# Performance work log

Measured on AMD Instinct MI355X. Metric: run time of the kernel, lower is better.

The kernel has to match this reference:

```python
import jax, jax.numpy as jnp
import numpy as np

NUM_EMBED = 8192
EMBED_DIM = 256


def setup_inputs() -> dict:
    key = jax.random.key(0)
    k1, k2 = jax.random.split(key)
    input_data = jax.random.normal(k1, (32, EMBED_DIM, 32, 32), dtype=jnp.float32)
    codebook = jax.random.normal(k2, (NUM_EMBED, EMBED_DIM), dtype=jnp.float32)
    return {"input_data": input_data, "codebook": codebook}


def reference(input_data, codebook):
    N, C, H, W = input_data.shape
    # NCHW -> NHWC -> [N*H*W, C]
    data = jnp.transpose(input_data, (0, 2, 3, 1)).reshape(-1, C)
    dist = (
        jnp.sum(data * data, axis=1, keepdims=True)          # [T, 1]
        - 2.0 * jnp.einsum("tc,kc->tk", data, codebook)      # [T, K]
        + jnp.sum(codebook * codebook, axis=1)[None, :]       # [1, K]
    )
    embed_ind = jnp.argmin(dist, axis=1)                      # [T]
    quantize = codebook[embed_ind]                            # [T, C] gather
    quantize_detach = data + jax.lax.stop_gradient(quantize - data)
    return quantize, quantize_detach, data
```

## Files before the change

kernel.cpp:

```cpp
#include <hip/hip_runtime.h>
#include <stdint.h>


#define T_TOT 32768
#define K_TOT 8192
#define CD    256
#define SPLITS 4
#define NSPLIT 2048
#define MT    64
#define NTI   32

typedef _Float16 h8 __attribute__((ext_vector_type(8)));
typedef _Float16 h4 __attribute__((ext_vector_type(4)));
typedef float f4 __attribute__((ext_vector_type(4)));
typedef unsigned long long u64;
typedef unsigned int u32;

#define WS_AP    0u
#define WS_BP    16777216u
#define WS_E2    20971520u
#define WS_E2B   21004288u
#define WS_CAND  21037056u
#define WS_NEED  23265280u

__device__ __forceinline__ u64 shfl_xor_u64(u64 v, int off, int w) {
  unsigned lo = (unsigned)v, hi = (unsigned)(v >> 32);
  lo = __shfl_xor(lo, off, w);
  hi = __shfl_xor(hi, off, w);
  return ((u64)hi << 32) | lo;
}
__device__ __forceinline__ u64 umin64(u64 a, u64 b) { return a < b ? a : b; }
__device__ __forceinline__ u64 umax64(u64 a, u64 b) { return a < b ? b : a; }
__device__ __forceinline__ u32 umin32(u32 a, u32 b) { return a < b ? a : b; }
__device__ __forceinline__ u32 umax32(u32 a, u32 b) { return a < b ? b : a; }

__device__ __forceinline__ void gll16(const void* g, void* l) {
  __builtin_amdgcn_global_load_lds(
      (const __attribute__((address_space(1))) void*)g,
      (__attribute__((address_space(3))) void*)l, 16, 0, 0);
}

__device__ __forceinline__ void stage_b(const _Float16* __restrict__ gsrc,
                                        _Float16* ldst, int lane) {
  #pragma unroll
  for (int kk = 0; kk < 8; ++kk)
    gll16(gsrc + kk * 512 + lane * 8, ldst + kk * 512);
}



__global__ __launch_bounds__(256) void cvt_data_kernel(
    const float* __restrict__ in, _Float16* __restrict__ Ap,
    float* __restrict__ out3) {
  __shared__ float Ds[32][257];
  const int tid = threadIdx.x;
  const int t0 = blockIdx.x * 32;
  const int nbase = (t0 >> 10) << 18;
  const int tin = t0 & 1023;
  #pragma unroll
  for (int p = 0; p < 8; ++p) {
    const int id = p * 256 + tid;
    const int cc = id >> 3, t4 = (id & 7) * 4;
    const float4 v = *(const float4*)(in + nbase + cc * 1024 + tin + t4);
    Ds[t4 + 0][cc] = v.x;
    Ds[t4 + 1][cc] = v.y;
    Ds[t4 + 2][cc] = v.z;
    Ds[t4 + 3][cc] = v.w;
  }
  __syncthreads();
  const u64 g0 = (u64)(t0 >> 4);
  #pragma unroll
  for (int p = 0; p < 4; ++p) {
    const int id = p * 256 + tid;
    const int gl = id >> 9, kk = (id >> 6) & 7, l = id & 63;
    const int row = gl * 16 + (l & 15);
    const int c0 = kk * 32 + (l >> 4) * 8;
    h8 hv;
    #pragma unroll
    for (int j = 0; j < 8; ++j) hv[j] = (_Float16)(-Ds[row][c0 + j]);
    *(h8*)(Ap + ((g0 + (u64)gl) * 8 + kk) * 512 + (u64)l * 8) = hv;
  }
  #pragma unroll 8
  for (int tt = 0; tt < 32; ++tt)
    out3[(u64)(t0 + tt) * CD + tid] = Ds[tt][tid];
}

__global__ __launch_bounds__(256) void cvt_cb_kernel(
    const float* __restrict__ cb, _Float16* __restrict__ Bp,
    float* __restrict__ e2, float* __restrict__ e2b) {
  __shared__ float Cs[16][260];
  const int tid = threadIdx.x;
  const int g = blockIdx.x;
  #pragma unroll
  for (int r = 0; r < 16; ++r)
    Cs[r][tid] = cb[((u64)g * 16 + r) * 256 + tid];
  __syncthreads();
  const int w = tid >> 6, lane = tid & 63;
  #pragma unroll
  for (int rr = 0; rr < 4; ++rr) {
    const int row = w * 4 + rr;
    const float4 v = *(const float4*)&Cs[row][lane * 4];
    float s = v.x * v.x + v.y * v.y + v.z * v.z + v.w * v.w;
    #pragma unroll
    for (int off = 32; off >= 1; off >>= 1) s += __shfl_xor(s, off, 64);
    if (lane == 0) {
      e2[g * 16 + row] = s;
      e2b[g * 16 + row] = 0.5f * s + 256.0f;
    }
  }
  #pragma unroll
  for (int p = 0; p < 2; ++p) {
    const int id = p * 256 + tid;
    const int kk = id >> 6, l = id & 63;
    const int row = l & 15, c0 = kk * 32 + (l >> 4) * 8;
    h8 hv;
    #pragma unroll
    for (int j = 0; j < 8; ++j) hv[j] = (_Float16)Cs[row][c0 + j];
    *(h8*)(Bp + ((u64)g * 8 + kk) * 512 + (u64)l * 8) = hv;
  }
}

__global__ __launch_bounds__(256, 2) void screen_kernel(
    const _Float16* __restrict__ Ap, const _Float16* __restrict__ Bp,
    const float* __restrict__ e2b, u64* __restrict__ cand) {
  __shared__ __align__(16) _Float16 bsm[4][2][4096];
  __shared__ __align__(16) float e2s[2048];

  const int tid = threadIdx.x;
  const int lane = tid & 63;
  const int w = __builtin_amdgcn_readfirstlane(tid >> 6);
  const int q = lane >> 4;
  const int c15 = lane & 15;

  const int x = blockIdx.x & 7;
  const int m = blockIdx.x >> 3;
  const int split = x >> 1;
  const int bm = m * 2 + (x & 1);
  const int t0 = bm * MT;
  const int n0s = split * NSPLIT;

  const h8* ap = (const h8*)Ap + (u64)(t0 >> 4) * 512 + lane;
  h8 af[4][8];
  #pragma unroll
  for (int mi = 0; mi < 4; ++mi)
    #pragma unroll
    for (int kk = 0; kk < 8; ++kk)
      af[mi][kk] = ap[(mi * 8 + kk) * 64];

  const _Float16* bg = Bp + ((u64)(n0s >> 4) + (u64)w) * 4096;
  stage_b(bg, &bsm[w][0][0], lane);
  stage_b(bg + 16384, &bsm[w][1][0], lane);
  gll16(e2b + n0s + w * 512 + lane * 4, e2s + w * 512);
  gll16(e2b + n0s + w * 512 + 256 + lane * 4, e2s + w * 512 + 256);

  u32 m1[16], m2[16];
  #pragma unroll
  for (int r = 0; r < 16; ++r) { m1[r] = 0xffffffffu; m2[r] = 0xffffffffu; }

  __syncthreads();

  #pragma unroll 2
  for (int nt = 0; nt < NTI; ++nt) {
    asm volatile("s_waitcnt vmcnt(8)" ::: "memory");
    _Float16* slot = &bsm[w][nt & 1][0];
    const float ev = e2s[nt * 64 + w * 16 + c15];
    h8 bf[8];
    #pragma unroll
    for (int kk = 0; kk < 8; ++kk)
      bf[kk] = *(const h8*)(slot + kk * 512 + lane * 8);

    f4 acc[4];
    #pragma unroll
    for (int mi = 0; mi < 4; ++mi) acc[mi] = (f4){ev, ev, ev, ev};
    __builtin_amdgcn_s_setprio(1);
    #pragma unroll
    for (int kk = 0; kk < 8; ++kk) {
      acc[0] = __builtin_amdgcn_mfma_f32_16x16x32_f16(af[0][kk], bf[kk], acc[0], 0, 0, 0);
      acc[1] = __builtin_amdgcn_mfma_f32_16x16x32_f16(af[1][kk], bf[kk], acc[1], 0, 0, 0);
      acc[2] = __builtin_amdgcn_mfma_f32_16x16x32_f16(af[2][kk], bf[kk], acc[2], 0, 0, 0);
      acc[3] = __builtin_amdgcn_mfma_f32_16x16x32_f16(af[3][kk], bf[kk], acc[3], 0, 0, 0);
    }
    __builtin_amdgcn_s_setprio(0);

    asm volatile("s_waitcnt lgkmcnt(0)" ::: "memory");
    __builtin_amdgcn_sched_barrier(0);
    const int g2 = (nt + 2 < NTI) ? nt + 2 : NTI - 1;
    stage_b(bg + (u64)g2 * 16384, slot, lane);

    #pragma unroll
    for (int mi = 0; mi < 4; ++mi)
      #pragma unroll
      for (int reg = 0; reg < 4; ++reg) {
        const int r = mi * 4 + reg;
        const u32 k = (__float_as_uint(acc[mi][reg]) & ~63u) | (u32)nt;
        const u32 hi = umax32(m1[r], k);
        m1[r] = umin32(m1[r], k);
        m2[r] = umin32(m2[r], hi);
      }
  }

  u64 P1[16], P2[16];
  #pragma unroll
  for (int r = 0; r < 16; ++r) {
    const u32 l1 = m1[r] & 63u, l2 = m2[r] & 63u;
    const u32 col1 = (u32)(n0s + (int)l1 * 64 + w * 16 + c15);
    const u32 col2 = (u32)(n0s + (int)l2 * 64 + w * 16 + c15);
    P1[r] = ((u64)m1[r] << 32) | col1;
    P2[r] = ((u64)m2[r] << 32) | col2;
  }
  #pragma unroll
  for (int st = 1; st < 16; st <<= 1) {
    #pragma unroll
    for (int r = 0; r < 16; ++r) {
      const u64 o1 = shfl_xor_u64(P1[r], st, 16);
      const u64 o2 = shfl_xor_u64(P2[r], st, 16);
      const u64 n1 = umin64(P1[r], o1);
      const u64 hi = umax64(P1[r], o1);
      P2[r] = umin64(hi, umin64(P2[r], o2));
      P1[r] = n1;
    }
  }
  __syncthreads();
  u64* mb = (u64*)&bsm[0][0][0];
  if (c15 == 0) {
    #pragma unroll
    for (int r = 0; r < 16; ++r) {
      const int mi = r >> 2, reg = r & 3;
      const int row = mi * 16 + q * 4 + reg;
      mb[(w * 64 + row) * 2 + 0] = P1[r];
      mb[(w * 64 + row) * 2 + 1] = P2[r];
    }
  }
  __syncthreads();
  if (tid < 64) {
    const u64 a1 = mb[(0 * 64 + tid) * 2], a2 = mb[(0 * 64 + tid) * 2 + 1];
    const u64 b1 = mb[(1 * 64 + tid) * 2], b2 = mb[(1 * 64 + tid) * 2 + 1];
    const u64 c1 = mb[(2 * 64 + tid) * 2], c2 = mb[(2 * 64 + tid) * 2 + 1];
    const u64 d1 = mb[(3 * 64 + tid) * 2], d2 = mb[(3 * 64 + tid) * 2 + 1];
    const u64 x1 = umin64(a1, b1);
    const u64 x2 = umin64(umax64(a1, b1), umin64(a2, b2));
    const u64 y1 = umin64(c1, d1);
    const u64 y2 = umin64(umax64(c1, d1), umin64(c2, d2));
    const u64 n1 = umin64(x1, y1);
    const u64 n2 = umin64(umax64(x1, y1), umin64(x2, y2));
    cand[(u64)(t0 + tid) * 8 + split * 2 + 0] = n1;
    cand[(u64)(t0 + tid) * 8 + split * 2 + 1] = n2;
  }
}

__global__ __launch_bounds__(256) void rescore_output_kernel(
    const float* __restrict__ cb, const float* __restrict__ e2,
    const u64* __restrict__ cand, float* __restrict__ out) {
  const int tid = threadIdx.x;
  const int w = tid >> 6, lane = tid & 63;
  const int t0 = blockIdx.x * 32 + w * 8;
  float* out1 = out;
  float* out2 = out + 8388608;
  const float* out3 = out + 16777216;
  #pragma unroll 1
  for (int s = 0; s < 8; ++s) {
    const int t = t0 + s;
    int colv = 0;
    if (lane < 8) colv = (int)(u32)cand[(u64)t * 8 + lane];
    const float4 x = *(const float4*)(out3 + (u64)t * CD + lane * 4);
    float bestd = 1e30f; int bestc = 0x7fffffff;
    #pragma unroll
    for (int j = 0; j < 8; ++j) {
      const int col = __shfl(colv, j, 64);
      const float4 e = *(const float4*)(cb + (u64)col * CD + lane * 4);
      float p4 = x.x * e.x + x.y * e.y + x.z * e.z + x.w * e.w;
      #pragma unroll
      for (int off = 32; off >= 1; off >>= 1) p4 += __shfl_xor(p4, off, 64);
      const float d = e2[col] - 2.0f * p4;
      if (d < bestd || (d == bestd && col < bestc)) { bestd = d; bestc = col; }
    }
    const float4 q4 = *(const float4*)(cb + (u64)bestc * CD + lane * 4);
    float4 qd4;
    qd4.x = x.x + (q4.x - x.x);
    qd4.y = x.y + (q4.y - x.y);
    qd4.z = x.z + (q4.z - x.z);
    qd4.w = x.w + (q4.w - x.w);
    const u64 o = (u64)t * CD + lane * 4;
    *(float4*)(out1 + o) = q4;
    *(float4*)(out2 + o) = qd4;
  }
}


__global__ __launch_bounds__(256) void norms_kernel(const float* __restrict__ in,
                                                    const float* __restrict__ cb,
                                                    float* __restrict__ e2,
                                                    float* __restrict__ x2) {
  const int b = blockIdx.x;
  const int tid = threadIdx.x;
  if (b < 2048) {
    const int wave = tid >> 6, lane = tid & 63;
    const int row = b * 4 + wave;
    const float4 v = *(const float4*)(cb + row * CD + lane * 4);
    float s = v.x * v.x + v.y * v.y + v.z * v.z + v.w * v.w;
    #pragma unroll
    for (int off = 32; off >= 1; off >>= 1) s += __shfl_down(s, off, 64);
    if (lane == 0) e2[row] = s;
  } else {
    const int t = (b - 2048) * 256 + tid;
    const float* p = in + ((t >> 10) << 18) + (t & 1023);
    float s = 0.f;
    #pragma unroll 8
    for (int c = 0; c < CD; ++c) { const float v = p[c << 10]; s += v * v; }
    x2[t] = s;
  }
}

__global__ __launch_bounds__(256) void dist_argmin_kernel(
    const float* __restrict__ in, const float* __restrict__ cb,
    const float* __restrict__ e2, const float* __restrict__ x2,
    u64* __restrict__ packed) {
  __shared__ __align__(16) float As_[32][128];
  __shared__ __align__(16) float Bs_[32][128];
  const int tid = threadIdx.x;
  const int tx = tid & 15, ty = tid >> 4;
  const int tb = blockIdx.x & 255;
  const int ks = blockIdx.x >> 8;
  const int t0 = tb * 128;
  const int nbase = (t0 >> 10) << 18;
  const int tin = t0 & 1023;
  float xi[8];
  #pragma unroll
  for (int i = 0; i < 8; ++i)
    xi[i] = x2[t0 + ty * 4 + (i & 3) + ((i >> 2) << 6)];
  u64 best[8];
  #pragma unroll
  for (int i = 0; i < 8; ++i) best[i] = ~0ull;
  for (int kt = 0; kt < 32; ++kt) {
    const int k0 = ks * 4096 + kt * 128;
    float acc[8][8];
    #pragma unroll
    for (int i = 0; i < 8; ++i)
      #pragma unroll
      for (int j = 0; j < 8; ++j) acc[i][j] = 0.f;
    float ej[8];
    #pragma unroll
    for (int j = 0; j < 8; ++j)
      ej[j] = e2[k0 + tx * 4 + (j & 3) + ((j >> 2) << 6)];
    for (int ch = 0; ch < 8; ++ch) {
      const int c0 = ch * 32;
      #pragma unroll
      for (int p = 0; p < 4; ++p) {
        const int l = p * 1024 + tid * 4;
        const int cc = l >> 7, tt = l & 127;
        *(float4*)&As_[cc][tt] =
            *(const float4*)(in + nbase + (c0 + cc) * 1024 + tin + tt);
      }
      #pragma unroll
      for (int p = 0; p < 4; ++p) {
        const int ix = p * 256 + tid;
        const int kk = ix >> 3, cs = (ix & 7) * 4;
        const float4 v = *(const float4*)(cb + (k0 + kk) * CD + c0 + cs);
        Bs_[cs + 0][kk] = v.x; Bs_[cs + 1][kk] = v.y;
        Bs_[cs + 2][kk] = v.z; Bs_[cs + 3][kk] = v.w;
      }
      __syncthreads();
      #pragma unroll
      for (int cc = 0; cc < 32; ++cc) {
        const float4 a0 = *(const float4*)&As_[cc][ty * 4];
        const float4 a1 = *(const float4*)&As_[cc][64 + ty * 4];
        const float4 b0 = *(const float4*)&Bs_[cc][tx * 4];
        const float4 b1 = *(const float4*)&Bs_[cc][64 + tx * 4];
        const float a[8]  = {a0.x, a0.y, a0.z, a0.w, a1.x, a1.y, a1.z, a1.w};
        const float bb[8] = {b0.x, b0.y, b0.z, b0.w, b1.x, b1.y, b1.z, b1.w};
        #pragma unroll
        for (int i = 0; i < 8; ++i)
          #pragma unroll
          for (int j = 0; j < 8; ++j)
            acc[i][j] += a[i] * bb[j];
      }
      __syncthreads();
    }
    #pragma unroll
    for (int i = 0; i < 8; ++i) {
      u64 m = best[i];
      #pragma unroll
      for (int j = 0; j < 8; ++j) {
        const float dist = (xi[i] - 2.0f * acc[i][j]) + ej[j];
        const int kidx = k0 + tx * 4 + (j & 3) + ((j >> 2) << 6);
        const u64 pk = ((u64)__float_as_uint(dist) << 32) | (unsigned)kidx;
        m = pk < m ? pk : m;
      }
      best[i] = m;
    }
  }
  #pragma unroll
  for (int i = 0; i < 8; ++i) {
    u64 m = best[i];
    #pragma unroll
    for (int off = 8; off >= 1; off >>= 1) {
      const u64 o = shfl_xor_u64(m, off, 16);
      m = o < m ? o : m;
    }
    if (tx == 0)
      atomicMin(&packed[t0 + ty * 4 + (i & 3) + ((i >> 2) << 6)], m);
  }
}

__global__ __launch_bounds__(256) void output_kernel(
    const float* __restrict__ in, const float* __restrict__ cb,
    const u64* __restrict__ packed, float* __restrict__ out) {
  __shared__ float Ds[32][257];
  __shared__ int idxs[32];
  const int tid = threadIdx.x;
  const int t0 = blockIdx.x * 32;
  const int nbase = (t0 >> 10) << 18;
  const int tin = t0 & 1023;
  if (tid < 32) idxs[tid] = (int)(packed[t0 + tid] & 0xffffffffull);
  #pragma unroll 8
  for (int p = 0; p < 32; ++p) {
    const int lin = p * 256 + tid;
    const int cc = lin >> 5, tt = lin & 31;
    Ds[tt][cc] = in[nbase + cc * 1024 + tin + tt];
  }
  __syncthreads();
  float* out1 = out;
  float* out2 = out + 8388608;
  float* out3 = out + 16777216;
  for (int tt = 0; tt < 32; ++tt) {
    const float d = Ds[tt][tid];
    const int k = idxs[tt];
    const float q = cb[k * CD + tid];
    const float qd = d + (q - d);
    const int o = (t0 + tt) * CD + tid;
    out1[o] = q;
    out2[o] = qd;
    out3[o] = d;
  }
}

extern "C" void kernel_launch(void* const* d_in, const int* in_sizes, int n_in,
                              void* d_out, int out_size, void* d_ws, size_t ws_size,
                              hipStream_t stream) {
  const float* in = (const float*)d_in[0];
  const float* cb = (const float*)d_in[1];
  float* out = (float*)d_out;

  if (ws_size >= WS_NEED) {
    _Float16* Ap = (_Float16*)((char*)d_ws + WS_AP);
    _Float16* Bp = (_Float16*)((char*)d_ws + WS_BP);
    float* e2  = (float*)((char*)d_ws + WS_E2);
    float* e2b = (float*)((char*)d_ws + WS_E2B);
    u64* cand  = (u64*)((char*)d_ws + WS_CAND);
    float* out3 = out + 16777216;

    cvt_data_kernel<<<T_TOT / 32, 256, 0, stream>>>(in, Ap, out3);
    cvt_cb_kernel<<<K_TOT / 16, 256, 0, stream>>>(cb, Bp, e2, e2b);
    screen_kernel<<<(T_TOT / MT) * SPLITS, 256, 0, stream>>>(Ap, Bp, e2b, cand);
    rescore_output_kernel<<<T_TOT / 32, 256, 0, stream>>>(cb, e2, cand, out);
  } else {
    u64* packed = (u64*)d_ws;
    float* e2 = (float*)((char*)d_ws + 262144);
    float* x2 = (float*)((char*)d_ws + 294912);
    (void)hipMemsetAsync(packed, 0xFF, T_TOT * sizeof(u64), stream);
    norms_kernel<<<2176, 256, 0, stream>>>(in, cb, e2, x2);
    dist_argmin_kernel<<<512, 256, 0, stream>>>(in, cb, e2, x2, packed);
    output_kernel<<<T_TOT / 32, 256, 0, stream>>>(in, cb, packed, out);
  }
}
```

Before: 329.7 us.

## Merge prep kernels and fuse rescore into screen via last-block counter

The two conversion kernels become one launch whose blocks split into data-transpose and codebook-conversion roles. The separate rescore/output kernel is removed: each screen block bumps a per-row-tile atomic counter, and the last of the four split blocks for that tile re-scores the candidates and writes the outputs. This cuts launches and inter-kernel gaps, at the cost of a memset for the counters, extra fences, and the rescore tail running on only a quarter of the screen blocks.

```diff
diff --git a/kernel.cpp b/kernel.cpp
--- a/kernel.cpp
+++ b/kernel.cpp
@@ -11,7 +11,6 @@
 #define NTI   32
 
 typedef _Float16 h8 __attribute__((ext_vector_type(8)));
-typedef _Float16 h4 __attribute__((ext_vector_type(4)));
 typedef float f4 __attribute__((ext_vector_type(4)));
 typedef unsigned long long u64;
 typedef unsigned int u32;
@@ -21,6 +20,7 @@
 #define WS_E2    20971520u
 #define WS_E2B   21004288u
 #define WS_CAND  21037056u
+#define WS_CTR   23134208u
 #define WS_NEED  23265280u
 
 __device__ __forceinline__ u64 shfl_xor_u64(u64 v, int off, int w) {
@@ -49,82 +49,84 @@
 
 
 
-__global__ __launch_bounds__(256) void cvt_data_kernel(
-    const float* __restrict__ in, _Float16* __restrict__ Ap,
+__global__ __launch_bounds__(256) void prep_kernel(
+    const float* __restrict__ in, const float* __restrict__ cb,
+    _Float16* __restrict__ Ap, _Float16* __restrict__ Bp,
+    float* __restrict__ e2, float* __restrict__ e2b,
     float* __restrict__ out3) {
-  __shared__ float Ds[32][257];
+  __shared__ float S[32][257];
   const int tid = threadIdx.x;
-  const int t0 = blockIdx.x * 32;
-  const int nbase = (t0 >> 10) << 18;
-  const int tin = t0 & 1023;
-  #pragma unroll
-  for (int p = 0; p < 8; ++p) {
-    const int id = p * 256 + tid;
-    const int cc = id >> 3, t4 = (id & 7) * 4;
-    const float4 v = *(const float4*)(in + nbase + cc * 1024 + tin + t4);
-    Ds[t4 + 0][cc] = v.x;
-    Ds[t4 + 1][cc] = v.y;
-    Ds[t4 + 2][cc] = v.z;
-    Ds[t4 + 3][cc] = v.w;
-  }
-  __syncthreads();
-  const u64 g0 = (u64)(t0 >> 4);
-  #pragma unroll
-  for (int p = 0; p < 4; ++p) {
-    const int id = p * 256 + tid;
-    const int gl = id >> 9, kk = (id >> 6) & 7, l = id & 63;
-    const int row = gl * 16 + (l & 15);
-    const int c0 = kk * 32 + (l >> 4) * 8;
-    h8 hv;
-    #pragma unroll
-    for (int j = 0; j < 8; ++j) hv[j] = (_Float16)(-Ds[row][c0 + j]);
-    *(h8*)(Ap + ((g0 + (u64)gl) * 8 + kk) * 512 + (u64)l * 8) = hv;
-  }
-  #pragma unroll 8
-  for (int tt = 0; tt < 32; ++tt)
-    out3[(u64)(t0 + tt) * CD + tid] = Ds[tt][tid];
-}
-
-__global__ __launch_bounds__(256) void cvt_cb_kernel(
-    const float* __restrict__ cb, _Float16* __restrict__ Bp,
-    float* __restrict__ e2, float* __restrict__ e2b) {
-  __shared__ float Cs[16][260];
-  const int tid = threadIdx.x;
-  const int g = blockIdx.x;
-  #pragma unroll
-  for (int r = 0; r < 16; ++r)
-    Cs[r][tid] = cb[((u64)g * 16 + r) * 256 + tid];
-  __syncthreads();
-  const int w = tid >> 6, lane = tid & 63;
-  #pragma unroll
-  for (int rr = 0; rr < 4; ++rr) {
-    const int row = w * 4 + rr;
-    const float4 v = *(const float4*)&Cs[row][lane * 4];
-    float s = v.x * v.x + v.y * v.y + v.z * v.z + v.w * v.w;
-    #pragma unroll
-    for (int off = 32; off >= 1; off >>= 1) s += __shfl_xor(s, off, 64);
-    if (lane == 0) {
-      e2[g * 16 + row] = s;
-      e2b[g * 16 + row] = 0.5f * s + 256.0f;
-    }
-  }
-  #pragma unroll
-  for (int p = 0; p < 2; ++p) {
-    const int id = p * 256 + tid;
-    const int kk = id >> 6, l = id & 63;
-    const int row = l & 15, c0 = kk * 32 + (l >> 4) * 8;
-    h8 hv;
-    #pragma unroll
-    for (int j = 0; j < 8; ++j) hv[j] = (_Float16)Cs[row][c0 + j];
-    *(h8*)(Bp + ((u64)g * 8 + kk) * 512 + (u64)l * 8) = hv;
+  if (blockIdx.x < 1024) {
+    const int t0 = blockIdx.x * 32;
+    const int nbase = (t0 >> 10) << 18;
+    const int tin = t0 & 1023;
+    #pragma unroll
+    for (int p = 0; p < 8; ++p) {
+      const int id = p * 256 + tid;
+      const int cc = id >> 3, t4 = (id & 7) * 4;
+      const float4 v = *(const float4*)(in + nbase + cc * 1024 + tin + t4);
+      S[t4 + 0][cc] = v.x;
+      S[t4 + 1][cc] = v.y;
+      S[t4 + 2][cc] = v.z;
+      S[t4 + 3][cc] = v.w;
+    }
+    __syncthreads();
+    const u64 g0 = (u64)(t0 >> 4);
+    #pragma unroll
+    for (int p = 0; p < 4; ++p) {
+      const int id = p * 256 + tid;
+      const int gl = id >> 9, kk = (id >> 6) & 7, l = id & 63;
+      const int row = gl * 16 + (l & 15);
+      const int c0 = kk * 32 + (l >> 4) * 8;
+      h8 hv;
+      #pragma unroll
+      for (int j = 0; j < 8; ++j) hv[j] = (_Float16)(-S[row][c0 + j]);
+      *(h8*)(Ap + ((g0 + (u64)gl) * 8 + kk) * 512 + (u64)l * 8) = hv;
+    }
+    #pragma unroll 8
+    for (int tt = 0; tt < 32; ++tt)
+      out3[(u64)(t0 + tt) * CD + tid] = S[tt][tid];
+  } else {
+    const int g = blockIdx.x - 1024;
+    float (*Cs)[260] = (float(*)[260])&S[0][0];
+    #pragma unroll
+    for (int r = 0; r < 16; ++r)
+      Cs[r][tid] = cb[((u64)g * 16 + r) * 256 + tid];
+    __syncthreads();
+    const int w = tid >> 6, lane = tid & 63;
+    #pragma unroll
+    for (int rr = 0; rr < 4; ++rr) {
+      const int row = w * 4 + rr;
+      const float4 v = *(const float4*)&Cs[row][lane * 4];
+      float s = v.x * v.x + v.y * v.y + v.z * v.z + v.w * v.w;
+      #pragma unroll
+      for (int off = 32; off >= 1; off >>= 1) s += __shfl_xor(s, off, 64);
+      if (lane == 0) {
+        e2[g * 16 + row] = s;
+        e2b[g * 16 + row] = 0.5f * s + 256.0f;
+      }
+    }
+    #pragma unroll
+    for (int p = 0; p < 2; ++p) {
+      const int id = p * 256 + tid;
+      const int kk = id >> 6, l = id & 63;
+      const int row = l & 15, c0 = kk * 32 + (l >> 4) * 8;
+      h8 hv;
+      #pragma unroll
+      for (int j = 0; j < 8; ++j) hv[j] = (_Float16)Cs[row][c0 + j];
+      *(h8*)(Bp + ((u64)g * 8 + kk) * 512 + (u64)l * 8) = hv;
+    }
   }
 }
 
 __global__ __launch_bounds__(256, 2) void screen_kernel(
     const _Float16* __restrict__ Ap, const _Float16* __restrict__ Bp,
-    const float* __restrict__ e2b, u64* __restrict__ cand) {
+    const float* __restrict__ cbf, const float* __restrict__ e2b,
+    const float* __restrict__ e2x, u64* __restrict__ cand,
+    int* __restrict__ ctr, float* outp) {
   __shared__ __align__(16) _Float16 bsm[4][2][4096];
   __shared__ __align__(16) float e2s[2048];
+  __shared__ int lastf;
 
   const int tid = threadIdx.x;
   const int lane = tid & 63;
@@ -246,40 +248,41 @@
     cand[(u64)(t0 + tid) * 8 + split * 2 + 0] = n1;
     cand[(u64)(t0 + tid) * 8 + split * 2 + 1] = n2;
   }
-}
-
-__global__ __launch_bounds__(256) void rescore_output_kernel(
-    const float* __restrict__ cb, const float* __restrict__ e2,
-    const u64* __restrict__ cand, float* __restrict__ out) {
-  const int tid = threadIdx.x;
-  const int w = tid >> 6, lane = tid & 63;
-  const int t0 = blockIdx.x * 32 + w * 8;
-  float* out1 = out;
-  float* out2 = out + 8388608;
-  const float* out3 = out + 16777216;
+
+  __threadfence();
+  __syncthreads();
+  if (tid == 0) lastf = (atomicAdd(ctr + bm, 1) == SPLITS - 1) ? 1 : 0;
+  __syncthreads();
+  if (!lastf) return;
+  __threadfence();
+
+  float* out1 = outp;
+  float* out2 = outp + 8388608;
+  const float* x3 = outp + 16777216;
   #pragma unroll 1
-  for (int s = 0; s < 8; ++s) {
-    const int t = t0 + s;
+  for (int s = 0; s < 16; ++s) {
+    const int t = t0 + w * 16 + s;
     int colv = 0;
-    if (lane < 8) colv = (int)(u32)cand[(u64)t * 8 + lane];
-    const float4 x = *(const float4*)(out3 + (u64)t * CD + lane * 4);
+    if (lane < 8)
+      colv = (int)(u32)*((volatile const u64*)cand + (u64)t * 8 + lane);
+    const float4 xv = *(const float4*)(x3 + (u64)t * CD + lane * 4);
     float bestd = 1e30f; int bestc = 0x7fffffff;
     #pragma unroll
     for (int j = 0; j < 8; ++j) {
       const int col = __shfl(colv, j, 64);
-      const float4 e = *(const float4*)(cb + (u64)col * CD + lane * 4);
-      float p4 = x.x * e.x + x.y * e.y + x.z * e.z + x.w * e.w;
+      const float4 e = *(const float4*)(cbf + (u64)col * CD + lane * 4);
+      float p4 = xv.x * e.x + xv.y * e.y + xv.z * e.z + xv.w * e.w;
       #pragma unroll
       for (int off = 32; off >= 1; off >>= 1) p4 += __shfl_xor(p4, off, 64);
-      const float d = e2[col] - 2.0f * p4;
+      const float d = e2x[col] - 2.0f * p4;
       if (d < bestd || (d == bestd && col < bestc)) { bestd = d; bestc = col; }
     }
-    const float4 q4 = *(const float4*)(cb + (u64)bestc * CD + lane * 4);
+    const float4 q4 = *(const float4*)(cbf + (u64)bestc * CD + lane * 4);
     float4 qd4;
-    qd4.x = x.x + (q4.x - x.x);
-    qd4.y = x.y + (q4.y - x.y);
-    qd4.z = x.z + (q4.z - x.z);
-    qd4.w = x.w + (q4.w - x.w);
+    qd4.x = xv.x + (q4.x - xv.x);
+    qd4.y = xv.y + (q4.y - xv.y);
+    qd4.z = xv.z + (q4.z - xv.z);
+    qd4.w = xv.w + (q4.w - xv.w);
     const u64 o = (u64)t * CD + lane * 4;
     *(float4*)(out1 + o) = q4;
     *(float4*)(out2 + o) = qd4;
@@ -447,12 +450,13 @@
     float* e2  = (float*)((char*)d_ws + WS_E2);
     float* e2b = (float*)((char*)d_ws + WS_E2B);
     u64* cand  = (u64*)((char*)d_ws + WS_CAND);
+    int* ctr   = (int*)((char*)d_ws + WS_CTR);
     float* out3 = out + 16777216;
 
-    cvt_data_kernel<<<T_TOT / 32, 256, 0, stream>>>(in, Ap, out3);
-    cvt_cb_kernel<<<K_TOT / 16, 256, 0, stream>>>(cb, Bp, e2, e2b);
-    screen_kernel<<<(T_TOT / MT) * SPLITS, 256, 0, stream>>>(Ap, Bp, e2b, cand);
-    rescore_output_kernel<<<T_TOT / 32, 256, 0, stream>>>(cb, e2, cand, out);
+    (void)hipMemsetAsync(ctr, 0, 512 * sizeof(int), stream);
+    prep_kernel<<<1536, 256, 0, stream>>>(in, cb, Ap, Bp, e2, e2b, out3);
+    screen_kernel<<<(T_TOT / MT) * SPLITS, 256, 0, stream>>>(
+        Ap, Bp, cb, e2b, e2, cand, ctr, out);
   } else {
     u64* packed = (u64*)d_ws;
     float* e2 = (float*)((char*)d_ws + 262144);
```

Measured after the change: 880.7 us. 2.67x slower.
